# Kernel optimization log

Measured on AMD Instinct MI355X. Metric: run time of the kernel, lower is better.

The kernel has to match this reference:

```python
import jax, jax.numpy as jnp
import numpy as np

D = 256
H = 8
DIM = D // H
NL = 8  # number of layers
LAYER_NAMES = ["self", "cross", "self", "cross", "self", "cross", "self", "cross"]
EPS_ATTN = 1e-6
EPS_LN = 1e-5


def setup_inputs() -> dict:
    key = jax.random.key(0)
    ks = jax.random.split(key, 16)
    B, L = 8, 4800
    s = 1.0 / np.sqrt(D)
    inp = {
        "desc0": jax.random.normal(ks[0], (B, L, D), jnp.float32),
        "desc1": jax.random.normal(ks[1], (B, L, D), jnp.float32),
        "mask0": jnp.ones((B, L), jnp.float32),
        "mask1": jnp.ones((B, L), jnp.float32),
        # shared LinearAttention params (one instance reused by all layers)
        "Wq": jax.random.normal(ks[2], (D, D), jnp.float32) * s,
        "bq": jnp.zeros((D,), jnp.float32),
        "Wk": jax.random.normal(ks[3], (D, D), jnp.float32) * s,
        "bk": jnp.zeros((D,), jnp.float32),
        "Wv": jax.random.normal(ks[4], (D, D), jnp.float32) * s,
        "bv": jnp.zeros((D,), jnp.float32),
        "Wm": jax.random.normal(ks[5], (D, D), jnp.float32) * s,
        "bm": jnp.zeros((D,), jnp.float32),
        # per-layer MLP (no bias) and layernorm params, stacked over layers
        "w1": jax.random.normal(ks[6], (NL, D, 2 * D), jnp.float32) * s,
        "w2": jax.random.normal(ks[7], (NL, 2 * D, D), jnp.float32) * (1.0 / np.sqrt(2 * D)),
        "g1": jnp.ones((NL, D), jnp.float32),
        "b1": jnp.zeros((NL, D), jnp.float32),
        "g2": jnp.ones((NL, D), jnp.float32),
        "b2": jnp.zeros((NL, D), jnp.float32),
    }
    return inp


def _layernorm(x, g, b):
    mu = jnp.mean(x, axis=-1, keepdims=True)
    var = jnp.mean(jnp.square(x - mu), axis=-1, keepdims=True)
    return (x - mu) * jax.lax.rsqrt(var + EPS_LN) * g + b


def _linear_attention(q_in, k_in, v_in, qmask, kmask, Wq, bq, Wk, bk, Wv, bv, Wm, bm):
    B, L, _ = q_in.shape
    Q = (q_in @ Wq + bq).reshape(B, -1, H, DIM)
    K = (k_in @ Wk + bk).reshape(B, -1, H, DIM)
    V = (v_in @ Wv + bv).reshape(B, -1, H, DIM)
    Q = jax.nn.elu(Q) + 1.0
    K = jax.nn.elu(K) + 1.0
    Q = Q * qmask[:, :, None, None]
    K = K * kmask[:, :, None, None]
    V = V * kmask[:, :, None, None]
    KV = jnp.einsum("nshd,nshm->nhmd", K, V)          # [B,H,DIM,DIM]
    Z = 1.0 / (jnp.einsum("nlhd,nhd->nlh", Q, K.sum(axis=1)) + EPS_ATTN)
    out = jnp.einsum("nlhd,nhmd,nlh->nlhm", Q, KV, Z)  # [B,L,H,DIM]
    return out.reshape(B, L, D) @ Wm + bm


def _layer(x, source, xmask, smask, Wq, bq, Wk, bk, Wv, bv, Wm, bm, w1, w2, g1, b1, g2, b2):
    msg = _linear_attention(x, source, source, xmask, smask, Wq, bq, Wk, bk, Wv, bv, Wm, bm)
    msg = _layernorm(msg, g1, b1)
    msg = jax.nn.relu(msg @ w1) @ w2
    msg = _layernorm(msg, g2, b2)
    return x + msg


def reference(desc0, desc1, mask0, mask1, Wq, bq, Wk, bk, Wv, bv, Wm, bm, w1, w2, g1, b1, g2, b2):
    attn = (Wq, bq, Wk, bk, Wv, bv, Wm, bm)
    for i, name in enumerate(LAYER_NAMES):
        lp = (w1[i], w2[i], g1[i], b1[i], g2[i], b2[i])
        if name == "self":
            desc0 = _layer(desc0, desc0, mask0, mask0, *attn, *lp)
            desc1 = _layer(desc1, desc1, mask1, mask1, *attn, *lp)
        else:
            desc0 = _layer(desc0, desc1, mask0, mask1, *attn, *lp)
            desc1 = _layer(desc1, desc0, mask1, mask0, *attn, *lp)
    return (desc0, desc1)
```

## Files before the change

### kernel.cpp

```cpp
#include <hip/hip_runtime.h>
#include <hip/hip_bf16.h>

typedef __attribute__((ext_vector_type(8))) short short8;
typedef __attribute__((ext_vector_type(4))) float f32x4;

#define NROWS 38400
#define LSEQ 4800
#define BATCH 8
#define NHEAD 8
#define QKV_LD 768

__device__ inline float b2f(ushort u) {
  union { ushort s; __hip_bfloat16 h; } c;
  c.s = u;
  return __bfloat162float(c.h);
}
__device__ inline ushort f2b(float f) {
  union { ushort s; __hip_bfloat16 h; } c;
  c.h = __float2bfloat16(f);
  return c.s;
}

__device__ inline void gll16(const void* g, void* l) {
  __builtin_amdgcn_global_load_lds(
      (const __attribute__((address_space(1))) void*)g,
      (__attribute__((address_space(3))) void*)l, 16, 0, 0);
}

__global__ __launch_bounds__(256) void transpose_bf16(
    const float* __restrict__ src, __hip_bfloat16* __restrict__ dst, int R, int C) {
  src += (size_t)blockIdx.z * R * C;
  dst += (size_t)blockIdx.z * R * C;
  __shared__ float tile[32][33];
  int bx = blockIdx.x, by = blockIdx.y;
  int tx = threadIdx.x & 31, ty = threadIdx.x >> 5;
  for (int rr = ty; rr < 32; rr += 8)
    tile[rr][tx] = src[(long)(by * 32 + rr) * C + bx * 32 + tx];
  __syncthreads();
  for (int rr = ty; rr < 32; rr += 8)
    dst[(long)(bx * 32 + rr) * R + by * 32 + tx] = __float2bfloat16(tile[tx][rr]);
}

__global__ __launch_bounds__(256) void init_x(
    const float* __restrict__ d0, const float* __restrict__ d1,
    float* __restrict__ outF, __hip_bfloat16* __restrict__ X0b,
    __hip_bfloat16* __restrict__ X1b, long n4) {
  long i = (long)blockIdx.x * 256 + threadIdx.x;
  if (i < n4) {
    float4 a = ((const float4*)d0)[i];
    float4 b = ((const float4*)d1)[i];
    ((float4*)outF)[i] = a;
    ((float4*)outF)[n4 + i] = b;
    ushort4 ua = {f2b(a.x), f2b(a.y), f2b(a.z), f2b(a.w)};
    ushort4 ub = {f2b(b.x), f2b(b.y), f2b(b.z), f2b(b.w)};
    ((ushort4*)X0b)[i] = ua;
    ((ushort4*)X1b)[i] = ub;
  }
}

__global__ __launch_bounds__(256) void gemm_qkv(
    const __hip_bfloat16* __restrict__ A, const __hip_bfloat16* __restrict__ Bt,
    __hip_bfloat16* __restrict__ C, int col0,
    const float* __restrict__ bq, const float* __restrict__ bk,
    const float* __restrict__ bv, const float* __restrict__ mq,
    const float* __restrict__ mkv) {
  __shared__ alignas(16) char smem[128 * 136 * 2];
  __hip_bfloat16 (*As)[64] = (__hip_bfloat16(*)[64])smem;
  __hip_bfloat16 (*Bs)[64] = (__hip_bfloat16(*)[64])(smem + 128 * 64 * 2);
  ushort (*Cs)[136] = (ushort(*)[136])smem;

  int tid = threadIdx.x;
  int wave = tid >> 6, lane = tid & 63;
  int wm = wave & 1, wn = wave >> 1;
  int quad = lane >> 4, l16 = lane & 15;
  long mbase = (long)blockIdx.y * 128;
  int nbase = blockIdx.x * 128;

  int srow = lane >> 3;
  int sck = (lane & 7) ^ srow;
  int cx = l16 & 7;

  f32x4 acc[4][4];
#pragma unroll
  for (int i = 0; i < 4; i++)
#pragma unroll
    for (int j = 0; j < 4; j++) acc[i][j] = (f32x4){0.f, 0.f, 0.f, 0.f};

  for (int kt = 0; kt < 256; kt += 64) {
    __syncthreads();
#pragma unroll
    for (int i = 0; i < 4; i++) {
      int r0 = wave * 32 + i * 8;
      gll16(A + (mbase + r0 + srow) * 256 + kt + sck * 8, &As[r0][0]);
      gll16(Bt + (long)(nbase + r0 + srow) * 256 + kt + sck * 8, &Bs[r0][0]);
    }
    __syncthreads();
#pragma unroll
    for (int ks = 0; ks < 64; ks += 32) {
      short8 af[4], bfr[4];
      int ch = ((ks >> 3) + quad) ^ cx;
#pragma unroll
      for (int mt = 0; mt < 4; mt++)
        af[mt] = *(const short8*)&As[wm * 64 + mt * 16 + l16][ch * 8];
#pragma unroll
      for (int nt = 0; nt < 4; nt++)
        bfr[nt] = *(const short8*)&Bs[wn * 64 + nt * 16 + l16][ch * 8];
#pragma unroll
      for (int mt = 0; mt < 4; mt++)
#pragma unroll
        for (int nt = 0; nt < 4; nt++)
          acc[mt][nt] = __builtin_amdgcn_mfma_f32_16x16x32_bf16(
              af[mt], bfr[nt], acc[mt][nt], 0, 0, 0);
    }
  }

  __syncthreads();
  int gc0 = col0 + nbase;
#pragma unroll
  for (int nt = 0; nt < 4; nt++) {
    int colt = wn * 64 + nt * 16 + l16;
    int gcol = gc0 + colt;
    int seg = gcol >> 8;
    int ci = gcol & 255;
    float bvv = (seg == 0) ? bq[ci] : (seg == 1) ? bk[ci] : bv[ci];
    const float* mask = (seg == 0) ? mq : mkv;
    bool doelu = seg < 2;
#pragma unroll
    for (int mt = 0; mt < 4; mt++) {
      int rowt0 = wm * 64 + mt * 16 + quad * 4;
#pragma unroll
      for (int r = 0; r < 4; r++) {
        int rowt = rowt0 + r;
        float v = acc[mt][nt][r] + bvv;
        if (doelu) v = v > 0.f ? v + 1.f : __expf(v);
        v *= mask[mbase + rowt];
        Cs[rowt][colt] = f2b(v);
      }
    }
  }
  __syncthreads();
#pragma unroll
  for (int it = 0; it < 8; it++) {
    int idx = tid + it * 256;
    int row = idx >> 4, c = idx & 15;
    uint4 v = *(const uint4*)&Cs[row][c * 8];
    *(uint4*)(C + (mbase + row) * (long)QKV_LD + gc0 + c * 8) = v;
  }
}

__global__ __launch_bounds__(512) void tail_fused(
    const __hip_bfloat16* __restrict__ A, const __hip_bfloat16* __restrict__ WmT,
    const __hip_bfloat16* __restrict__ w1T, const __hip_bfloat16* __restrict__ w2T,
    const float* __restrict__ bm,
    const float* __restrict__ g1, const float* __restrict__ b1,
    const float* __restrict__ g2, const float* __restrict__ b2,
    float* __restrict__ outF, __hip_bfloat16* __restrict__ Xb) {
  __shared__ alignas(16) char smem[152064];
  ushort* Msu  = (ushort*)(smem + 81920);
  ushort* H1u  = (ushort*)(smem + 114688);
  float* pS  = (float*)(smem + 147456);
  float* pS2 = (float*)(smem + 149504);
  float* muA = (float*)(smem + 151552);
  float* rsA = (float*)(smem + 151808);

  int tid = threadIdx.x;
  int wave = tid >> 6, lane = tid & 63;
  int quad = lane >> 4, l16 = lane & 15;
  long mbase = (long)blockIdx.x * 64;
  int srow = lane >> 3;
  int sck = (lane & 7) ^ srow;
  int cx = l16 & 7;
  int swz = cx * 8;

  f32x4 accA[4][2], accB[4][2], accC[4][2];
#pragma unroll
  for (int i = 0; i < 4; i++)
#pragma unroll
    for (int j = 0; j < 2; j++) {
      accA[i][j] = (f32x4){0.f, 0.f, 0.f, 0.f};
      accC[i][j] = (f32x4){0.f, 0.f, 0.f, 0.f};
    }

  auto stageA = [&](int b, int kt) {
    char* base = smem + b * 40960;
    __hip_bfloat16 (*As)[64] = (__hip_bfloat16(*)[64])base;
    __hip_bfloat16 (*Bs)[64] = (__hip_bfloat16(*)[64])(base + 8192);
    gll16(A + (mbase + wave * 8 + srow) * 256 + kt + sck * 8, &As[wave * 8][0]);
#pragma unroll
    for (int j = 0; j < 4; j++) {
      int r0 = wave * 32 + j * 8;
      gll16(WmT + (r0 + srow) * 256 + kt + sck * 8, &Bs[r0][0]);
    }
  };
  auto stageB = [&](int b, int half, int kt) {
    __hip_bfloat16 (*Bs)[64] = (__hip_bfloat16(*)[64])(smem + b * 40960 + 8192);
#pragma unroll
    for (int j = 0; j < 4; j++) {
      int r0 = wave * 32 + j * 8;
      gll16(w1T + (half * 256 + r0 + srow) * 256 + kt + sck * 8, &Bs[r0][0]);
    }
  };
  auto stageC = [&](int b, int half, int kt) {
    __hip_bfloat16 (*Bs)[64] = (__hip_bfloat16(*)[64])(smem + b * 40960 + 8192);
#pragma unroll
    for (int j = 0; j < 4; j++) {
      int r0 = wave * 32 + j * 8;
      gll16(w2T + (r0 + srow) * 512L + half * 256 + kt + sck * 8, &Bs[r0][0]);
    }
  };

  auto computeA = [&](int b) {
    char* base = smem + b * 40960;
    __hip_bfloat16 (*As)[64] = (__hip_bfloat16(*)[64])base;
    __hip_bfloat16 (*Bs)[64] = (__hip_bfloat16(*)[64])(base + 8192);
#pragma unroll
    for (int ks = 0; ks < 64; ks += 32) {
      short8 af[4], bfr[2];
      int ch = ((ks >> 3) + quad) ^ cx;
#pragma unroll
      for (int mt = 0; mt < 4; mt++)
        af[mt] = *(const short8*)&As[mt * 16 + l16][ch * 8];
#pragma unroll
      for (int nt = 0; nt < 2; nt++)
        bfr[nt] = *(const short8*)&Bs[wave * 32 + nt * 16 + l16][ch * 8];
#pragma unroll
      for (int mt = 0; mt < 4; mt++)
#pragma unroll
        for (int nt = 0; nt < 2; nt++)
          accA[mt][nt] = __builtin_amdgcn_mfma_f32_16x16x32_bf16(
              af[mt], bfr[nt], accA[mt][nt], 0, 0, 0);
    }
  };
  auto computeB = [&](int b, int kt) {
    __hip_bfloat16 (*Bs)[64] = (__hip_bfloat16(*)[64])(smem + b * 40960 + 8192);
#pragma unroll
    for (int ks = 0; ks < 64; ks += 32) {
      short8 af[4], bfr[2];
      int ch = ((ks >> 3) + quad) ^ cx;
      int mcol = (kt + ks + quad * 8) ^ swz;
#pragma unroll
      for (int mt = 0; mt < 4; mt++)
        af[mt] = *(const short8*)&Msu[(mt * 16 + l16) * 256 + mcol];
#pragma unroll
      for (int nt = 0; nt < 2; nt++)
        bfr[nt] = *(const short8*)&Bs[wave * 32 + nt * 16 + l16][ch * 8];
#pragma unroll
      for (int mt = 0; mt < 4; mt++)
#pragma unroll
        for (int nt = 0; nt < 2; nt++)
          accB[mt][nt] = __builtin_amdgcn_mfma_f32_16x16x32_bf16(
              af[mt], bfr[nt], accB[mt][nt], 0, 0, 0);
    }
  };
  auto computeC = [&](int b, int kt) {
    __hip_bfloat16 (*Bs)[64] = (__hip_bfloat16(*)[64])(smem + b * 40960 + 8192);
#pragma unroll
    for (int ks = 0; ks < 64; ks += 32) {
      short8 af[4], bfr[2];
      int ch = ((ks >> 3) + quad) ^ cx;
      int hcol = (kt + ks + quad * 8) ^ swz;
#pragma unroll
      for (int mt = 0; mt < 4; mt++)
        af[mt] = *(const short8*)&H1u[(mt * 16 + l16) * 256 + hcol];
#pragma unroll
      for (int nt = 0; nt < 2; nt++)
        bfr[nt] = *(const short8*)&Bs[wave * 32 + nt * 16 + l16][ch * 8];
#pragma unroll
      for (int mt = 0; mt < 4; mt++)
#pragma unroll
        for (int nt = 0; nt < 2; nt++)
          accC[mt][nt] = __builtin_amdgcn_mfma_f32_16x16x32_bf16(
              af[mt], bfr[nt], accC[mt][nt], 0, 0, 0);
    }
  };

#define PIPE_SYNC                                      \
  asm volatile("s_waitcnt vmcnt(0)" ::: "memory");     \
  __builtin_amdgcn_sched_barrier(0);                   \
  __builtin_amdgcn_s_barrier();

  int cb = 0;
  stageA(0, 0);
  PIPE_SYNC
#pragma unroll
  for (int t = 0; t < 4; t++) {
    if (t < 3) stageA(cb ^ 1, (t + 1) * 64); else stageB(cb ^ 1, 0, 0);
    computeA(cb);
    PIPE_SYNC
    cb ^= 1;
  }
  float br[2], gr[2], blr[2];
#pragma unroll
  for (int nt = 0; nt < 2; nt++) {
    int gcol = wave * 32 + nt * 16 + l16;
    br[nt] = bm[gcol];
    gr[nt] = g1[gcol];
    blr[nt] = b1[gcol];
  }
#pragma unroll
  for (int mt = 0; mt < 4; mt++)
#pragma unroll
    for (int r = 0; r < 4; r++) {
      float s = 0.f, s2 = 0.f;
#pragma unroll
      for (int nt = 0; nt < 2; nt++) {
        float v = accA[mt][nt][r] + br[nt];
        s += v;
        s2 += v * v;
      }
      s += __shfl_xor(s, 1);  s2 += __shfl_xor(s2, 1);
      s += __shfl_xor(s, 2);  s2 += __shfl_xor(s2, 2);
      s += __shfl_xor(s, 4);  s2 += __shfl_xor(s2, 4);
      s += __shfl_xor(s, 8);  s2 += __shfl_xor(s2, 8);
      if (l16 == 0) {
        int row = mt * 16 + quad * 4 + r;
        pS[wave * 64 + row] = s;
        pS2[wave * 64 + row] = s2;
      }
    }
  __syncthreads();
  if (tid < 64) {
    float S = 0.f, S2 = 0.f;
#pragma unroll
    for (int w = 0; w < 8; w++) { S += pS[w * 64 + tid]; S2 += pS2[w * 64 + tid]; }
    float mu = S * (1.f / 256.f);
    float var = S2 * (1.f / 256.f) - mu * mu;
    muA[tid] = mu;
    rsA[tid] = rsqrtf(var + 1e-5f);
  }
  __syncthreads();
#pragma unroll
  for (int mt = 0; mt < 4; mt++)
#pragma unroll
    for (int r = 0; r < 4; r++) {
      int row = mt * 16 + quad * 4 + r;
      float mu = muA[row], rs = rsA[row];
      int rsw = (row & 7) * 8;
#pragma unroll
      for (int nt = 0; nt < 2; nt++) {
        int col = wave * 32 + nt * 16 + l16;
        float v = accA[mt][nt][r] + br[nt];
        Msu[row * 256 + (col ^ rsw)] = f2b((v - mu) * rs * gr[nt] + blr[nt]);
      }
    }
  __syncthreads();

#pragma unroll
  for (int half = 0; half < 2; half++) {
#pragma unroll
    for (int i = 0; i < 4; i++)
#pragma unroll
      for (int j = 0; j < 2; j++) accB[i][j] = (f32x4){0.f, 0.f, 0.f, 0.f};
#pragma unroll
    for (int t = 0; t < 4; t++) {
      if (t < 3) stageB(cb ^ 1, half, (t + 1) * 64); else stageC(cb ^ 1, half, 0);
      computeB(cb, t * 64);
      PIPE_SYNC
      cb ^= 1;
    }
#pragma unroll
    for (int mt = 0; mt < 4; mt++)
#pragma unroll
      for (int r = 0; r < 4; r++) {
        int row = mt * 16 + quad * 4 + r;
        int rsw = (row & 7) * 8;
#pragma unroll
        for (int nt = 0; nt < 2; nt++) {
          int col = wave * 32 + nt * 16 + l16;
          float v = accB[mt][nt][r];
          H1u[row * 256 + (col ^ rsw)] = f2b(v > 0.f ? v : 0.f);
        }
      }
    __syncthreads();
#pragma unroll
    for (int t = 0; t < 4; t++) {
      if (t < 3) stageC(cb ^ 1, half, (t + 1) * 64);
      else if (half == 0) stageB(cb ^ 1, 1, 0);
      computeC(cb, t * 64);
      PIPE_SYNC
      cb ^= 1;
    }
  }

  float g2r[2], b2r[2];
#pragma unroll
  for (int nt = 0; nt < 2; nt++) {
    int gcol = wave * 32 + nt * 16 + l16;
    g2r[nt] = g2[gcol];
    b2r[nt] = b2[gcol];
  }
#pragma unroll
  for (int mt = 0; mt < 4; mt++)
#pragma unroll
    for (int r = 0; r < 4; r++) {
      float s = 0.f, s2 = 0.f;
#pragma unroll
      for (int nt = 0; nt < 2; nt++) {
        float v = accC[mt][nt][r];
        s += v;
        s2 += v * v;
      }
      s += __shfl_xor(s, 1);  s2 += __shfl_xor(s2, 1);
      s += __shfl_xor(s, 2);  s2 += __shfl_xor(s2, 2);
      s += __shfl_xor(s, 4);  s2 += __shfl_xor(s2, 4);
      s += __shfl_xor(s, 8);  s2 += __shfl_xor(s2, 8);
      if (l16 == 0) {
        int row = mt * 16 + quad * 4 + r;
        pS[wave * 64 + row] = s;
        pS2[wave * 64 + row] = s2;
      }
    }
  __syncthreads();
  if (tid < 64) {
    float S = 0.f, S2 = 0.f;
#pragma unroll
    for (int w = 0; w < 8; w++) { S += pS[w * 64 + tid]; S2 += pS2[w * 64 + tid]; }
    float mu = S * (1.f / 256.f);
    float var = S2 * (1.f / 256.f) - mu * mu;
    muA[tid] = mu;
    rsA[tid] = rsqrtf(var + 1e-5f);
  }
  __syncthreads();
  ushort* Xsu = Msu;
#pragma unroll
  for (int mt = 0; mt < 4; mt++)
#pragma unroll
    for (int r = 0; r < 4; r++) {
      int row = mt * 16 + quad * 4 + r;
      float mu = muA[row], rs = rsA[row];
#pragma unroll
      for (int nt = 0; nt < 2; nt++) {
        int gcol = wave * 32 + nt * 16 + l16;
        float ln = (accC[mt][nt][r] - mu) * rs * g2r[nt] + b2r[nt];
        float* op = outF + (mbase + row) * 256 + gcol;
        float rr = *op + ln;
        *op = rr;
        Xsu[row * 256 + gcol] = f2b(rr);
      }
    }
  __syncthreads();
#pragma unroll
  for (int it = 0; it < 4; it++) {
    int idx = tid + it * 512;
    int row = idx >> 5, c = idx & 31;
    uint4 v = *(const uint4*)&Xsu[row * 256 + c * 8];
    *(uint4*)(Xb + (mbase + row) * 256L + c * 8) = v;
  }
#undef PIPE_SYNC
}

__global__ __launch_bounds__(256) void kv_reduce(
    const __hip_bfloat16* __restrict__ QKV, float* __restrict__ KV,
    float* __restrict__ Ksum) {
  int b = blockIdx.x, h = blockIdx.y, c = blockIdx.z;
  __shared__ float Kl[32][40], Vl[32][40];
  int t = threadIdx.x;
  int lrow = t >> 3, le = (t & 7) * 4;
  int d = t >> 3, mg = t & 7;
  float a0 = 0.f, a1 = 0.f, a2 = 0.f, a3 = 0.f, ks = 0.f;
  int base = c * 480;
  for (int st = 0; st < 15; st++) {
    int s0 = base + st * 32;
    __syncthreads();
    {
      long n = (long)b * LSEQ + s0 + lrow;
      ushort4 ku = *(const ushort4*)(QKV + n * QKV_LD + 256 + h * 32 + le);
      ushort4 vu = *(const ushort4*)(QKV + n * QKV_LD + 512 + h * 32 + le);
      float4 kf = {b2f(ku.x), b2f(ku.y), b2f(ku.z), b2f(ku.w)};
      float4 vf = {b2f(vu.x), b2f(vu.y), b2f(vu.z), b2f(vu.w)};
      *(float4*)&Kl[lrow][le] = kf;
      *(float4*)&Vl[lrow][le] = vf;
    }
    __syncthreads();
#pragma unroll
    for (int ss = 0; ss < 32; ss++) {
      float kd = Kl[ss][d];
      float4 v4 = *(const float4*)&Vl[ss][mg * 4];
      a0 += kd * v4.x; a1 += kd * v4.y; a2 += kd * v4.z; a3 += kd * v4.w;
      if (mg == 0) ks += kd;
    }
  }
  int bh = b * 8 + h;
  float* p = KV + ((long)bh * 32 + d) * 32 + mg * 4;
  atomicAdd(&p[0], a0); atomicAdd(&p[1], a1);
  atomicAdd(&p[2], a2); atomicAdd(&p[3], a3);
  if (mg == 0) atomicAdd(&Ksum[bh * 32 + d], ks);
}

__global__ __launch_bounds__(256) void attn_out(
    const __hip_bfloat16* __restrict__ QKV, const float* __restrict__ KV,
    const float* __restrict__ Ksum, __hip_bfloat16* __restrict__ O) {
  int b = blockIdx.y, h = blockIdx.z;
  int bh = b * 8 + h;
  __shared__ float KVl[32][36];
  int t = threadIdx.x;
  for (int i = t; i < 1024; i += 256) KVl[i >> 5][i & 31] = KV[((long)bh << 10) + i];
  int lane = t & 63, wave = t >> 6;
  int cg = lane & 7, rs = lane >> 3;
  float4 ksr = *(const float4*)&Ksum[bh * 32 + cg * 4];
  __syncthreads();

  int rowEnd = blockIdx.x * 192 + 192;
  for (int r = blockIdx.x * 192 + wave * 8 + rs; r < rowEnd; r += 32) {
    long n = (long)b * LSEQ + r;
    ushort4 qu = *(const ushort4*)(QKV + n * QKV_LD + h * 32 + cg * 4);
    float q0 = b2f(qu.x), q1 = b2f(qu.y), q2 = b2f(qu.z), q3 = b2f(qu.w);
    float den = q0 * ksr.x + q1 * ksr.y + q2 * ksr.z + q3 * ksr.w;
    den += __shfl_xor(den, 1);
    den += __shfl_xor(den, 2);
    den += __shfl_xor(den, 4);
    float s0 = 0.f, s1 = 0.f, s2 = 0.f, s3 = 0.f;
    int gbase = lane & ~7;
#pragma unroll
    for (int j = 0; j < 8; j++) {
      int src = gbase | j;
      float qa = __shfl(q0, src);
      float qb = __shfl(q1, src);
      float qc = __shfl(q2, src);
      float qd = __shfl(q3, src);
      float4 k0 = *(const float4*)&KVl[j * 4 + 0][cg * 4];
      float4 k1 = *(const float4*)&KVl[j * 4 + 1][cg * 4];
      float4 k2 = *(const float4*)&KVl[j * 4 + 2][cg * 4];
      float4 k3 = *(const float4*)&KVl[j * 4 + 3][cg * 4];
      s0 += qa * k0.x + qb * k1.x + qc * k2.x + qd * k3.x;
      s1 += qa * k0.y + qb * k1.y + qc * k2.y + qd * k3.y;
      s2 += qa * k0.z + qb * k1.z + qc * k2.z + qd * k3.z;
      s3 += qa * k0.w + qb * k1.w + qc * k2.w + qd * k3.w;
    }
    float inv = 1.0f / (den + 1e-6f);
    ushort4 ou = {f2b(s0 * inv), f2b(s1 * inv), f2b(s2 * inv), f2b(s3 * inv)};
    *(ushort4*)(O + n * 256 + h * 32 + cg * 4) = ou;
  }
}

extern "C" void kernel_launch(void* const* d_in, const int* in_sizes, int n_in,
                              void* d_out, int out_size, void* d_ws, size_t ws_size,
                              hipStream_t stream) {
  const float* desc0 = (const float*)d_in[0];
  const float* desc1 = (const float*)d_in[1];
  const float* mask0 = (const float*)d_in[2];
  const float* mask1 = (const float*)d_in[3];
  const float* Wq = (const float*)d_in[4];
  const float* bq = (const float*)d_in[5];
  const float* Wk = (const float*)d_in[6];
  const float* bk = (const float*)d_in[7];
  const float* Wv = (const float*)d_in[8];
  const float* bv = (const float*)d_in[9];
  const float* Wm = (const float*)d_in[10];
  const float* bm = (const float*)d_in[11];
  const float* w1 = (const float*)d_in[12];
  const float* w2 = (const float*)d_in[13];
  const float* g1 = (const float*)d_in[14];
  const float* b1 = (const float*)d_in[15];
  const float* g2 = (const float*)d_in[16];
  const float* b2 = (const float*)d_in[17];

  char* ws = (char*)d_ws;
  size_t used = 0;
  auto alloc = [&](size_t bytes) {
    char* p = ws + used;
    used += (bytes + 255) & ~(size_t)255;
    return p;
  };
  __hip_bfloat16* WqkvT = (__hip_bfloat16*)alloc((size_t)768 * 256 * 2);
  __hip_bfloat16* WmT = (__hip_bfloat16*)alloc(256 * 256 * 2);
  __hip_bfloat16* w1T = (__hip_bfloat16*)alloc((size_t)8 * 512 * 256 * 2);
  __hip_bfloat16* w2T = (__hip_bfloat16*)alloc((size_t)8 * 256 * 512 * 2);
  __hip_bfloat16* X0b = (__hip_bfloat16*)alloc((size_t)NROWS * 256 * 2);
  __hip_bfloat16* X1b = (__hip_bfloat16*)alloc((size_t)NROWS * 256 * 2);
  __hip_bfloat16* QKV = (__hip_bfloat16*)alloc((size_t)NROWS * QKV_LD * 2);
  __hip_bfloat16* Ab2 = (__hip_bfloat16*)alloc((size_t)2 * NROWS * 256 * 2);
  float* KVws = (float*)alloc((64 * 1024 + 64 * 32) * 4);
  float* Ksum = KVws + 64 * 1024;
  bool merged = used <= ws_size;

  transpose_bf16<<<dim3(8, 8, 1), 256, 0, stream>>>(Wq, WqkvT, 256, 256);
  transpose_bf16<<<dim3(8, 8, 1), 256, 0, stream>>>(Wk, WqkvT + 65536, 256, 256);
  transpose_bf16<<<dim3(8, 8, 1), 256, 0, stream>>>(Wv, WqkvT + 131072, 256, 256);
  transpose_bf16<<<dim3(8, 8, 1), 256, 0, stream>>>(Wm, WmT, 256, 256);
  transpose_bf16<<<dim3(16, 8, 8), 256, 0, stream>>>(w1, w1T, 256, 512);
  transpose_bf16<<<dim3(8, 16, 8), 256, 0, stream>>>(w2, w2T, 512, 256);

  long nElem = (long)NROWS * 256;
  long n4 = nElem / 4;
  init_x<<<(n4 + 255) / 256, 256, 0, stream>>>(desc0, desc1, (float*)d_out,
                                               X0b, X1b, n4);

  auto attn_stage = [&](const __hip_bfloat16* Xq, const __hip_bfloat16* Xkv,
                        const float* mq, const float* ms,
                        __hip_bfloat16* Oout, bool self) {
    if (self) {
      gemm_qkv<<<dim3(6, 300), 256, 0, stream>>>(Xq, WqkvT, QKV, 0,
                                                 bq, bk, bv, mq, ms);
    } else {
      gemm_qkv<<<dim3(2, 300), 256, 0, stream>>>(Xq, WqkvT, QKV, 0,
                                                 bq, bk, bv, mq, ms);
      gemm_qkv<<<dim3(4, 300), 256, 0, stream>>>(Xkv, WqkvT + 65536, QKV, 256,
                                                 bq, bk, bv, mq, ms);
    }
    hipMemsetAsync(KVws, 0, (64 * 1024 + 64 * 32) * 4, stream);
    kv_reduce<<<dim3(BATCH, NHEAD, 10), 256, 0, stream>>>(QKV, KVws, Ksum);
    attn_out<<<dim3(25, BATCH, NHEAD), 256, 0, stream>>>(QKV, KVws, Ksum, Oout);
  };

  auto tail = [&](int nblk, int i, float* oF, __hip_bfloat16* Xb) {
    tail_fused<<<nblk, 512, 0, stream>>>(
        Ab2, WmT, w1T + (size_t)i * 512 * 256, w2T + (size_t)i * 256 * 512,
        bm, g1 + i * 256, b1 + i * 256, g2 + i * 256, b2 + i * 256, oF, Xb);
  };

  auto self_pair = [&](int i) {
    attn_stage(X0b, X0b, mask0, mask0, Ab2, true);
    attn_stage(X1b, X1b, mask1, mask1, Ab2 + nElem, true);
    tail(2 * NROWS / 64, i, (float*)d_out, X0b);
  };

  auto layer_one = [&](int x, int s, int i) {
    __hip_bfloat16* Xx = x ? X1b : X0b;
    __hip_bfloat16* Xs = s ? X1b : X0b;
    const float* mx = x ? mask1 : mask0;
    const float* ms = s ? mask1 : mask0;
    attn_stage(Xx, Xs, mx, ms, Ab2, x == s);
    tail(NROWS / 64, i, (float*)d_out + (size_t)x * nElem, Xx);
  };

  for (int i = 0; i < 8; i++) {
    if (i % 2 == 0) {
      if (merged) {
        self_pair(i);
      } else {
        layer_one(0, 0, i);
        layer_one(1, 1, i);
      }
    } else {
      layer_one(0, 1, i);
      layer_one(1, 0, i);
    }
  }
}
```

Before: 3.071 ms.

## Read tail GEMM weights from global memory and shrink LDS for occupancy

Rewrites the fused tail kernel (Wm projection, LayerNorm, MLP, LayerNorm, residual) so weight fragments are loaded straight from global memory into registers instead of being staged through double-buffered LDS. The A tile is loaded once in full and reused as the hidden-activation buffer, cutting shared memory from about 149KB to about 69KB and adding a launch-bounds hint of 4 blocks. It also swizzles the bf16 output staging buffer to reduce bank conflicts. The cost is that weight loads no longer overlap with compute through a software pipeline, so global/L2 latency shows up in the MFMA loops, and the occupancy hint may force register spills.

```diff
diff --git a/kernel.cpp b/kernel.cpp
--- a/kernel.cpp
+++ b/kernel.cpp
@@ -148,31 +148,29 @@
   }
 }
 
-__global__ __launch_bounds__(512) void tail_fused(
+__global__ __launch_bounds__(512, 4) void tail_fused(
     const __hip_bfloat16* __restrict__ A, const __hip_bfloat16* __restrict__ WmT,
     const __hip_bfloat16* __restrict__ w1T, const __hip_bfloat16* __restrict__ w2T,
     const float* __restrict__ bm,
     const float* __restrict__ g1, const float* __restrict__ b1,
     const float* __restrict__ g2, const float* __restrict__ b2,
     float* __restrict__ outF, __hip_bfloat16* __restrict__ Xb) {
-  __shared__ alignas(16) char smem[152064];
-  ushort* Msu  = (ushort*)(smem + 81920);
-  ushort* H1u  = (ushort*)(smem + 114688);
-  float* pS  = (float*)(smem + 147456);
-  float* pS2 = (float*)(smem + 149504);
-  float* muA = (float*)(smem + 151552);
-  float* rsA = (float*)(smem + 151808);
+  __shared__ alignas(16) char smem[70144];
+  ushort* AsH = (ushort*)smem;
+  ushort* Msu = (ushort*)(smem + 32768);
+  float* pS  = (float*)(smem + 65536);
+  float* pS2 = (float*)(smem + 67584);
+  float* muA = (float*)(smem + 69632);
+  float* rsA = (float*)(smem + 69888);
 
   int tid = threadIdx.x;
   int wave = tid >> 6, lane = tid & 63;
   int quad = lane >> 4, l16 = lane & 15;
   long mbase = (long)blockIdx.x * 64;
-  int srow = lane >> 3;
-  int sck = (lane & 7) ^ srow;
   int cx = l16 & 7;
-  int swz = cx * 8;
-
-  f32x4 accA[4][2], accB[4][2], accC[4][2];
+  int rswL = cx * 8;
+
+  f32x4 accA[4][2], accC[4][2];
 #pragma unroll
   for (int i = 0; i < 4; i++)
 #pragma unroll
@@ -181,114 +179,39 @@
       accC[i][j] = (f32x4){0.f, 0.f, 0.f, 0.f};
     }
 
-  auto stageA = [&](int b, int kt) {
-    char* base = smem + b * 40960;
-    __hip_bfloat16 (*As)[64] = (__hip_bfloat16(*)[64])base;
-    __hip_bfloat16 (*Bs)[64] = (__hip_bfloat16(*)[64])(base + 8192);
-    gll16(A + (mbase + wave * 8 + srow) * 256 + kt + sck * 8, &As[wave * 8][0]);
+  {
+    int r2 = lane >> 5;
+    int c32 = lane & 31;
 #pragma unroll
     for (int j = 0; j < 4; j++) {
-      int r0 = wave * 32 + j * 8;
-      gll16(WmT + (r0 + srow) * 256 + kt + sck * 8, &Bs[r0][0]);
-    }
-  };
-  auto stageB = [&](int b, int half, int kt) {
-    __hip_bfloat16 (*Bs)[64] = (__hip_bfloat16(*)[64])(smem + b * 40960 + 8192);
-#pragma unroll
-    for (int j = 0; j < 4; j++) {
-      int r0 = wave * 32 + j * 8;
-      gll16(w1T + (half * 256 + r0 + srow) * 256 + kt + sck * 8, &Bs[r0][0]);
-    }
-  };
-  auto stageC = [&](int b, int half, int kt) {
-    __hip_bfloat16 (*Bs)[64] = (__hip_bfloat16(*)[64])(smem + b * 40960 + 8192);
-#pragma unroll
-    for (int j = 0; j < 4; j++) {
-      int r0 = wave * 32 + j * 8;
-      gll16(w2T + (r0 + srow) * 512L + half * 256 + kt + sck * 8, &Bs[r0][0]);
-    }
-  };
-
-  auto computeA = [&](int b) {
-    char* base = smem + b * 40960;
-    __hip_bfloat16 (*As)[64] = (__hip_bfloat16(*)[64])base;
-    __hip_bfloat16 (*Bs)[64] = (__hip_bfloat16(*)[64])(base + 8192);
-#pragma unroll
-    for (int ks = 0; ks < 64; ks += 32) {
-      short8 af[4], bfr[2];
-      int ch = ((ks >> 3) + quad) ^ cx;
-#pragma unroll
-      for (int mt = 0; mt < 4; mt++)
-        af[mt] = *(const short8*)&As[mt * 16 + l16][ch * 8];
+      int r0 = wave * 8 + j * 2;
+      int r = r0 + r2;
+      gll16(A + (mbase + r) * 256 + ((c32 ^ (r & 7)) * 8),
+            (char*)AsH + r0 * 512);
+    }
+  }
+  __syncthreads();
+
+#pragma unroll
+  for (int ks = 0; ks < 256; ks += 32) {
+    short8 af[4], bfr[2];
+#pragma unroll
+    for (int nt = 0; nt < 2; nt++) {
+      int n = wave * 32 + nt * 16 + l16;
+      bfr[nt] = *(const short8*)&WmT[n * 256 + ks + quad * 8];
+    }
+    int ch = ((ks >> 3) + quad) ^ cx;
+#pragma unroll
+    for (int mt = 0; mt < 4; mt++)
+      af[mt] = *(const short8*)&AsH[(mt * 16 + l16) * 256 + ch * 8];
+#pragma unroll
+    for (int mt = 0; mt < 4; mt++)
 #pragma unroll
       for (int nt = 0; nt < 2; nt++)
-        bfr[nt] = *(const short8*)&Bs[wave * 32 + nt * 16 + l16][ch * 8];
-#pragma unroll
-      for (int mt = 0; mt < 4; mt++)
-#pragma unroll
-        for (int nt = 0; nt < 2; nt++)
-          accA[mt][nt] = __builtin_amdgcn_mfma_f32_16x16x32_bf16(
-              af[mt], bfr[nt], accA[mt][nt], 0, 0, 0);
-    }
-  };
-  auto computeB = [&](int b, int kt) {
-    __hip_bfloat16 (*Bs)[64] = (__hip_bfloat16(*)[64])(smem + b * 40960 + 8192);
-#pragma unroll
-    for (int ks = 0; ks < 64; ks += 32) {
-      short8 af[4], bfr[2];
-      int ch = ((ks >> 3) + quad) ^ cx;
-      int mcol = (kt + ks + quad * 8) ^ swz;
-#pragma unroll
-      for (int mt = 0; mt < 4; mt++)
-        af[mt] = *(const short8*)&Msu[(mt * 16 + l16) * 256 + mcol];
-#pragma unroll
-      for (int nt = 0; nt < 2; nt++)
-        bfr[nt] = *(const short8*)&Bs[wave * 32 + nt * 16 + l16][ch * 8];
-#pragma unroll
-      for (int mt = 0; mt < 4; mt++)
-#pragma unroll
-        for (int nt = 0; nt < 2; nt++)
-          accB[mt][nt] = __builtin_amdgcn_mfma_f32_16x16x32_bf16(
-              af[mt], bfr[nt], accB[mt][nt], 0, 0, 0);
-    }
-  };
-  auto computeC = [&](int b, int kt) {
-    __hip_bfloat16 (*Bs)[64] = (__hip_bfloat16(*)[64])(smem + b * 40960 + 8192);
-#pragma unroll
-    for (int ks = 0; ks < 64; ks += 32) {
-      short8 af[4], bfr[2];
-      int ch = ((ks >> 3) + quad) ^ cx;
-      int hcol = (kt + ks + quad * 8) ^ swz;
-#pragma unroll
-      for (int mt = 0; mt < 4; mt++)
-        af[mt] = *(const short8*)&H1u[(mt * 16 + l16) * 256 + hcol];
-#pragma unroll
-      for (int nt = 0; nt < 2; nt++)
-        bfr[nt] = *(const short8*)&Bs[wave * 32 + nt * 16 + l16][ch * 8];
-#pragma unroll
-      for (int mt = 0; mt < 4; mt++)
-#pragma unroll
-        for (int nt = 0; nt < 2; nt++)
-          accC[mt][nt] = __builtin_amdgcn_mfma_f32_16x16x32_bf16(
-              af[mt], bfr[nt], accC[mt][nt], 0, 0, 0);
-    }
-  };
-
-#define PIPE_SYNC                                      \
-  asm volatile("s_waitcnt vmcnt(0)" ::: "memory");     \
-  __builtin_amdgcn_sched_barrier(0);                   \
-  __builtin_amdgcn_s_barrier();
-
-  int cb = 0;
-  stageA(0, 0);
-  PIPE_SYNC
-#pragma unroll
-  for (int t = 0; t < 4; t++) {
-    if (t < 3) stageA(cb ^ 1, (t + 1) * 64); else stageB(cb ^ 1, 0, 0);
-    computeA(cb);
-    PIPE_SYNC
-    cb ^= 1;
-  }
+        accA[mt][nt] = __builtin_amdgcn_mfma_f32_16x16x32_bf16(
+            af[mt], bfr[nt], accA[mt][nt], 0, 0, 0);
+  }
+
   float br[2], gr[2], blr[2];
 #pragma unroll
   for (int nt = 0; nt < 2; nt++) {
@@ -347,17 +270,32 @@
 
 #pragma unroll
   for (int half = 0; half < 2; half++) {
+    f32x4 accB[4][2];
 #pragma unroll
     for (int i = 0; i < 4; i++)
 #pragma unroll
       for (int j = 0; j < 2; j++) accB[i][j] = (f32x4){0.f, 0.f, 0.f, 0.f};
-#pragma unroll
-    for (int t = 0; t < 4; t++) {
-      if (t < 3) stageB(cb ^ 1, half, (t + 1) * 64); else stageC(cb ^ 1, half, 0);
-      computeB(cb, t * 64);
-      PIPE_SYNC
-      cb ^= 1;
-    }
+    const __hip_bfloat16* w1h = w1T + (size_t)half * 256 * 256;
+#pragma unroll
+    for (int ks = 0; ks < 256; ks += 32) {
+      short8 af[4], bfr[2];
+#pragma unroll
+      for (int nt = 0; nt < 2; nt++) {
+        int n = wave * 32 + nt * 16 + l16;
+        bfr[nt] = *(const short8*)&w1h[n * 256 + ks + quad * 8];
+      }
+      int pcol = (ks + quad * 8) ^ rswL;
+#pragma unroll
+      for (int mt = 0; mt < 4; mt++)
+        af[mt] = *(const short8*)&Msu[(mt * 16 + l16) * 256 + pcol];
+#pragma unroll
+      for (int mt = 0; mt < 4; mt++)
+#pragma unroll
+        for (int nt = 0; nt < 2; nt++)
+          accB[mt][nt] = __builtin_amdgcn_mfma_f32_16x16x32_bf16(
+              af[mt], bfr[nt], accB[mt][nt], 0, 0, 0);
+    }
+    __syncthreads();
 #pragma unroll
     for (int mt = 0; mt < 4; mt++)
 #pragma unroll
@@ -368,17 +306,28 @@
         for (int nt = 0; nt < 2; nt++) {
           int col = wave * 32 + nt * 16 + l16;
           float v = accB[mt][nt][r];
-          H1u[row * 256 + (col ^ rsw)] = f2b(v > 0.f ? v : 0.f);
+          AsH[row * 256 + (col ^ rsw)] = f2b(v > 0.f ? v : 0.f);
         }
       }
     __syncthreads();
 #pragma unroll
-    for (int t = 0; t < 4; t++) {
-      if (t < 3) stageC(cb ^ 1, half, (t + 1) * 64);
-      else if (half == 0) stageB(cb ^ 1, 1, 0);
-      computeC(cb, t * 64);
-      PIPE_SYNC
-      cb ^= 1;
+    for (int ks = 0; ks < 256; ks += 32) {
+      short8 af[4], bfr[2];
+#pragma unroll
+      for (int nt = 0; nt < 2; nt++) {
+        int n = wave * 32 + nt * 16 + l16;
+        bfr[nt] = *(const short8*)&w2T[n * 512 + half * 256 + ks + quad * 8];
+      }
+      int pcol = (ks + quad * 8) ^ rswL;
+#pragma unroll
+      for (int mt = 0; mt < 4; mt++)
+        af[mt] = *(const short8*)&AsH[(mt * 16 + l16) * 256 + pcol];
+#pragma unroll
+      for (int mt = 0; mt < 4; mt++)
+#pragma unroll
+        for (int nt = 0; nt < 2; nt++)
+          accC[mt][nt] = __builtin_amdgcn_mfma_f32_16x16x32_bf16(
+              af[mt], bfr[nt], accC[mt][nt], 0, 0, 0);
     }
   }
 
@@ -428,6 +377,7 @@
     for (int r = 0; r < 4; r++) {
       int row = mt * 16 + quad * 4 + r;
       float mu = muA[row], rs = rsA[row];
+      int qx = quad * 8;
 #pragma unroll
       for (int nt = 0; nt < 2; nt++) {
         int gcol = wave * 32 + nt * 16 + l16;
@@ -435,7 +385,7 @@
         float* op = outF + (mbase + row) * 256 + gcol;
         float rr = *op + ln;
         *op = rr;
-        Xsu[row * 256 + gcol] = f2b(rr);
+        Xsu[row * 256 + (gcol ^ qx)] = f2b(rr);
       }
     }
   __syncthreads();
@@ -443,10 +393,10 @@
   for (int it = 0; it < 4; it++) {
     int idx = tid + it * 512;
     int row = idx >> 5, c = idx & 31;
-    uint4 v = *(const uint4*)&Xsu[row * 256 + c * 8];
+    int pc = c ^ ((row >> 2) & 3);
+    uint4 v = *(const uint4*)&Xsu[row * 256 + pc * 8];
     *(uint4*)(Xb + (mbase + row) * 256L + c * 8) = v;
   }
-#undef PIPE_SYNC
 }
 
 __global__ __launch_bounds__(256) void kv_reduce(
```

Measured after the change: 3.700 ms. 1.2x slower.
